# Optimization experiments

Hardware: AMD Instinct MI355X
Metric: run time of the kernel (lower is better)

Reference implementation:

```python
import jax, jax.numpy as jnp
import numpy as np

TOP_K = 6
N_GROUP = 4
TOPK_GROUP = 2
ROUTED_SCALING = 2.5

T, H, E, I = 1024, 2048, 16, 704  # tokens, hidden, experts, expert ffn width
IS = 2 * I  # shared expert intermediate (n_shared_experts * moe_intermediate_size)


def setup_inputs() -> dict:
    key = jax.random.key(0)
    ks = jax.random.split(key, 6)
    s = 0.02
    return {
        "hidden_states": jax.random.normal(ks[0], (T, H), jnp.float32),
        "w_gate": jax.random.normal(ks[1], (H, E), jnp.float32) * s,
        "w_gate_up": jax.random.normal(ks[2], (E, H, 2 * I), jnp.float32) * s,
        "w_down": jax.random.normal(ks[3], (E, I, H), jnp.float32) * s,
        "w_shared_gate_up": jax.random.normal(ks[4], (H, 2 * IS), jnp.float32) * s,
        "w_shared_down": jax.random.normal(ks[5], (IS, H), jnp.float32) * s,
    }


def grouped_topk(scores, k, n_group, topk_group):
    # DeepSeek grouped top-k routing: pick topk_group expert groups by max
    # group score, mask out other groups, then top-k over remaining experts.
    t, e = scores.shape
    group_scores = scores.reshape(t, n_group, e // n_group).max(axis=-1)  # [T, G]
    _, gidx = jax.lax.top_k(group_scores, topk_group)                     # [T, kg]
    gmask = jax.nn.one_hot(gidx, n_group, dtype=scores.dtype).sum(axis=1)  # [T, G]
    smask = jnp.repeat(gmask, e // n_group, axis=1)                        # [T, E]
    masked = jnp.where(smask > 0, scores, 0.0)
    topk_w, topk_idx = jax.lax.top_k(masked, k)                            # [T, k]
    topk_w = topk_w / jnp.sum(topk_w, axis=-1, keepdims=True)              # renormalize
    return topk_w, topk_idx


def reference(hidden_states, w_gate, w_gate_up, w_down, w_shared_gate_up, w_shared_down):
    x = hidden_states                         # [T, H]
    t, e = x.shape[0], w_gate.shape[1]
    # router
    router_logits = x @ w_gate                # [T, E]
    scores = jax.nn.softmax(router_logits, axis=-1)
    topk_w, topk_idx = grouped_topk(scores, TOP_K, N_GROUP, TOPK_GROUP)
    combine = jnp.zeros((t, e), x.dtype).at[jnp.arange(t)[:, None], topk_idx].add(topk_w)
    # routed experts (dense-all-experts form, mathematically identical to dispatch)
    gu = jnp.einsum('th,ehi->tei', x, w_gate_up)        # [T, E, 2I]
    g, u = jnp.split(gu, 2, axis=-1)
    act = jax.nn.silu(g) * u                            # [T, E, I]
    act = act * combine[:, :, None]                     # apply routing weights
    routed = jnp.einsum('tei,eih->th', act, w_down) * ROUTED_SCALING
    # shared experts (SiLU gated MLP)
    sgu = x @ w_shared_gate_up
    sg, su = jnp.split(sgu, 2, axis=-1)
    shared = (jax.nn.silu(sg) * su) @ w_shared_down
    return routed + shared
```

## Files before the change

kernel.cpp:

```cpp
#include <hip/hip_runtime.h>

typedef unsigned short u16;
typedef u16 u16x8 __attribute__((ext_vector_type(8)));
typedef __bf16 bf16x8 __attribute__((ext_vector_type(8)));
typedef float f32x4 __attribute__((ext_vector_type(4)));

#define T_TOK 1024
#define H_DIM 2048
#define E_NUM 16
#define I_DIM 704
#define IS_DIM 1408

#define MFMA(a, b, c) __builtin_amdgcn_mfma_f32_16x16x32_bf16(a, b, c, 0, 0, 0)

__device__ __forceinline__ u16 f2bf(float f) {
  union { float f; unsigned u; } v; v.f = f;
  unsigned r = v.u + 0x7fffu + ((v.u >> 16) & 1u);
  return (u16)(r >> 16);
}

__device__ __forceinline__ void gload16(const void* g, void* l) {
  __builtin_amdgcn_global_load_lds(
      (const __attribute__((address_space(1))) unsigned int*)g,
      (__attribute__((address_space(3))) unsigned int*)l, 16, 0, 0);
}

__device__ __forceinline__ const char* lds_sw(const u16* base, int row, int kByte) {
  return (const char*)base + row * 128 + (kByte ^ ((row & 7) << 4));
}

__device__ __forceinline__ void transp64_body(const float* __restrict__ in,
                                              u16* __restrict__ outp, int R, int C,
                                              int cx, int ry, int z, char* SM) {
  float (*tile)[65] = (float(*)[65])SM;
  const size_t base = (size_t)z * (size_t)R * C;
  const int c0 = cx * 64, r0 = ry * 64;
  const int tid = threadIdx.x;
  const int c4 = (tid & 15) * 4, rb = tid >> 4;
#pragma unroll
  for (int i = 0; i < 4; ++i) {
    const int row = i * 16 + rb;
    const f32x4 v = *(const f32x4*)(in + base + (size_t)(r0 + row) * C + c0 + c4);
    tile[row][c4 + 0] = v[0];
    tile[row][c4 + 1] = v[1];
    tile[row][c4 + 2] = v[2];
    tile[row][c4 + 3] = v[3];
  }
  __syncthreads();
#pragma unroll
  for (int i = 0; i < 8; ++i) {
    const int idx = i * 256 + tid;
    const int oc = idx >> 5, pr = idx & 31;
    const unsigned lo = f2bf(tile[2 * pr][oc]);
    const unsigned hi = f2bf(tile[2 * pr + 1][oc]);
    *(unsigned*)&outp[base + (size_t)(c0 + oc) * R + r0 + 2 * pr] = lo | (hi << 16);
  }
}

__global__ __launch_bounds__(256) void router_k(const float* __restrict__ x,
                                                const float* __restrict__ wg,
                                                float* __restrict__ comb,
                                                u16* __restrict__ XB) {
  const int t = blockIdx.x;
  const int tid = threadIdx.x;
  const float* xr = x + (size_t)t * H_DIM;
  const int h0 = tid * 8;
  f32x4 a = *(const f32x4*)(xr + h0);
  f32x4 b = *(const f32x4*)(xr + h0 + 4);
  u16x8 o;
  o[0] = f2bf(a[0]); o[1] = f2bf(a[1]); o[2] = f2bf(a[2]); o[3] = f2bf(a[3]);
  o[4] = f2bf(b[0]); o[5] = f2bf(b[1]); o[6] = f2bf(b[2]); o[7] = f2bf(b[3]);
  *(u16x8*)(XB + (size_t)t * H_DIM + h0) = o;

  float acc[E_NUM];
#pragma unroll
  for (int e = 0; e < E_NUM; ++e) acc[e] = 0.f;
#pragma unroll
  for (int j = 0; j < 8; ++j) {
    const float xv = j < 4 ? a[j] : b[j - 4];
    const f32x4* wr = (const f32x4*)(wg + (size_t)(h0 + j) * E_NUM);
#pragma unroll
    for (int q = 0; q < 4; ++q) {
      f32x4 w4 = wr[q];
      acc[q * 4 + 0] += xv * w4[0];
      acc[q * 4 + 1] += xv * w4[1];
      acc[q * 4 + 2] += xv * w4[2];
      acc[q * 4 + 3] += xv * w4[3];
    }
  }
#pragma unroll
  for (int e = 0; e < E_NUM; ++e)
    for (int off = 32; off > 0; off >>= 1) acc[e] += __shfl_down(acc[e], off);
  __shared__ float part[4][E_NUM];
  if ((tid & 63) == 0) {
#pragma unroll
    for (int e = 0; e < E_NUM; ++e) part[tid >> 6][e] = acc[e];
  }
  __syncthreads();
  if (tid == 0) {
    float p[E_NUM];
    float mx = -1e30f;
    for (int e = 0; e < E_NUM; ++e) {
      p[e] = part[0][e] + part[1][e] + part[2][e] + part[3][e];
      mx = fmaxf(mx, p[e]);
    }
    float s = 0.f;
    for (int e = 0; e < E_NUM; ++e) { p[e] = __expf(p[e] - mx); s += p[e]; }
    const float invs = 1.f / s;
    for (int e = 0; e < E_NUM; ++e) p[e] *= invs;
    float gs[4];
    for (int g = 0; g < 4; ++g)
      gs[g] = fmaxf(fmaxf(p[4 * g], p[4 * g + 1]), fmaxf(p[4 * g + 2], p[4 * g + 3]));
    int g1 = 0;
    for (int g = 1; g < 4; ++g) if (gs[g] > gs[g1]) g1 = g;
    int g2 = -1;
    for (int g = 0; g < 4; ++g) {
      if (g == g1) continue;
      if (g2 < 0 || gs[g] > gs[g2]) g2 = g;
    }
    float m2[E_NUM], cw[E_NUM];
    for (int e = 0; e < E_NUM; ++e) {
      int g = e >> 2;
      m2[e] = (g == g1 || g == g2) ? p[e] : 0.f;
      cw[e] = 0.f;
    }
    float sum6 = 0.f;
    for (int k = 0; k < 6; ++k) {
      int bi = 0; float bv = -1.f;
      for (int e = 0; e < E_NUM; ++e)
        if (m2[e] > bv) { bv = m2[e]; bi = e; }
      cw[bi] = bv; sum6 += bv; m2[bi] = -2.f;
    }
    const float scale = 2.5f / sum6;
    for (int e = 0; e < E_NUM; ++e) comb[t * E_NUM + e] = cw[e] * scale;
  }
}

__global__ __launch_bounds__(256) void dispatch_k(const float* __restrict__ comb,
                                                  int* __restrict__ cnt,
                                                  int* __restrict__ tok) {
  const int e = blockIdx.x;
  const int tid = threadIdx.x;
  const int lane = tid & 63, wid = tid >> 6;
  __shared__ int wtot[4];
  int running = 0;
  for (int chunk = 0; chunk < T_TOK / 256; ++chunk) {
    const int t = chunk * 256 + tid;
    const bool sel = comb[t * E_NUM + e] > 0.f;
    unsigned long long mask = __ballot(sel);
    const int pre = __popcll(mask & ((1ull << lane) - 1ull));
    if (lane == 0) wtot[wid] = __popcll(mask);
    __syncthreads();
    int wbase = running;
    for (int w = 0; w < wid; ++w) wbase += wtot[w];
    if (sel) tok[e * T_TOK + wbase + pre] = t;
    running += wtot[0] + wtot[1] + wtot[2] + wtot[3];
    __syncthreads();
  }
  if (tid == 0) cnt[e] = running;
}

#define TGU_WGU_BLKS (22 * 32 * 16)
__global__ __launch_bounds__(256) void transp_gu_k(const float* __restrict__ wgu,
                                                   const float* __restrict__ wsgu,
                                                   u16* __restrict__ WGUT,
                                                   u16* __restrict__ WSGUT) {
  __shared__ __align__(16) char SM[16640];
  const int bid = blockIdx.x;
  if (bid < TGU_WGU_BLKS) {
    transp64_body(wgu, WGUT, H_DIM, 2 * I_DIM, bid % 22, (bid / 22) % 32, bid / 704, SM);
  } else {
    const int id = bid - TGU_WGU_BLKS;
    transp64_body(wsgu, WSGUT, H_DIM, 2 * IS_DIM, id % 44, id / 44, 0, SM);
  }
}

__device__ __forceinline__ void gu_body(
    const u16* __restrict__ A, const u16* __restrict__ Bt,
    const float* __restrict__ comb, const int* __restrict__ cnt,
    const int* __restrict__ tok, u16* __restrict__ outp,
    int gu_off, long long bt_e_stride, long long out_e_stride, int out_stride,
    int bx, int by, int e, char* SM) {
  const int M = cnt ? cnt[e] : T_TOK;
  const int m0 = by * 128;
  if (m0 >= M) return;
  u16* S = (u16*)SM;
  int* tokS = (int*)(SM + 32768);

  const int n0 = bx * 64;
  const u16* Bte = Bt + (size_t)e * bt_e_stride;
  const u16* Bgp = Bte + (size_t)n0 * H_DIM;
  const u16* Bup = Bte + (size_t)(gu_off + n0) * H_DIM;
  const int tid = threadIdx.x;
  const int w = tid >> 6, l = tid & 63;
  const int r8 = l >> 3;
  const int sk = ((l & 7) ^ r8) * 8;

  if (tid < 128) {
    const int m = m0 + tid;
    const int mc = m < M ? m : M - 1;
    tokS[tid] = tok ? tok[e * T_TOK + mc] : mc;
  }
  size_t arow[4];
#pragma unroll
  for (int j = 0; j < 4; ++j) {
    const int m = m0 + w * 32 + j * 8 + r8;
    const int mc = m < M ? m : M - 1;
    const int t = tok ? tok[e * T_TOK + mc] : mc;
    arow[j] = (size_t)t * H_DIM + sk;
  }

  const int wr = tid >> 7;
  const int wc = (tid >> 6) & 1;
  const int fr = l & 15;
  const int fg = l >> 4;

  const f32x4 zero = {0.f, 0.f, 0.f, 0.f};
  f32x4 accg[4][2], accu[4][2];
#pragma unroll
  for (int i = 0; i < 4; ++i)
#pragma unroll
    for (int j = 0; j < 2; ++j) { accg[i][j] = zero; accu[i][j] = zero; }

  for (int kt = 0; kt < H_DIM / 64; ++kt) {
    const int k0 = kt * 64;
#pragma unroll
    for (int j = 0; j < 4; ++j)
      gload16(A + arow[j] + k0, S + (w * 4 + j) * 512);
#pragma unroll
    for (int j = 0; j < 2; ++j) {
      const size_t br = (size_t)(w * 16 + j * 8 + r8) * H_DIM + sk + k0;
      gload16(Bgp + br, S + 8192 + (w * 2 + j) * 512);
      gload16(Bup + br, S + 12288 + (w * 2 + j) * 512);
    }
    __syncthreads();
    const u16* AsC = S;
    const u16* BgC = S + 8192;
    const u16* BuC = S + 12288;
#pragma unroll
    for (int kk = 0; kk < 2; ++kk) {
      const int kb = kk * 64 + fg * 16;
      bf16x8 af[4], bg[2], bu[2];
#pragma unroll
      for (int mi = 0; mi < 4; ++mi)
        af[mi] = *(const bf16x8*)lds_sw(AsC, wr * 64 + mi * 16 + fr, kb);
#pragma unroll
      for (int ni = 0; ni < 2; ++ni) {
        bg[ni] = *(const bf16x8*)lds_sw(BgC, wc * 32 + ni * 16 + fr, kb);
        bu[ni] = *(const bf16x8*)lds_sw(BuC, wc * 32 + ni * 16 + fr, kb);
      }
#pragma unroll
      for (int mi = 0; mi < 4; ++mi)
#pragma unroll
        for (int ni = 0; ni < 2; ++ni) {
          accg[mi][ni] = MFMA(af[mi], bg[ni], accg[mi][ni]);
          accu[mi][ni] = MFMA(af[mi], bu[ni], accu[mi][ni]);
        }
    }
    __syncthreads();
  }

  const int colb = n0 + wc * 32;
#pragma unroll
  for (int mi = 0; mi < 4; ++mi) {
#pragma unroll
    for (int r = 0; r < 4; ++r) {
      const int ml = wr * 64 + mi * 16 + fg * 4 + r;
      if (m0 + ml >= M) continue;
      const float wgt = comb ? comb[tokS[ml] * E_NUM + e] : 1.0f;
      const size_t rowoff = (size_t)e * out_e_stride + (size_t)(m0 + ml) * out_stride;
#pragma unroll
      for (int ni = 0; ni < 2; ++ni) {
        float g = accg[mi][ni][r];
        float u = accu[mi][ni][r];
        float sg = g / (1.f + __expf(-g));
        outp[rowoff + colb + ni * 16 + fr] = f2bf(sg * u * wgt);
      }
    }
  }
}

#define MG_GUR_BLKS (11 * 8 * 16)
#define MG_GUS_BLKS (22 * 8)
#define MG_TWD_BLKS (32 * 11 * 16)
#define MG_TWSD_BLKS (32 * 22)
__global__ __launch_bounds__(256, 4) void mega_k(
    const u16* __restrict__ XB, const u16* __restrict__ WGUT,
    const u16* __restrict__ WSGUT, const float* __restrict__ comb,
    const int* __restrict__ cnt, const int* __restrict__ tok,
    u16* __restrict__ ACTC, u16* __restrict__ ACTS,
    const float* __restrict__ wd, const float* __restrict__ wsd,
    u16* __restrict__ WDT, u16* __restrict__ WSDT) {
  __shared__ __align__(16) char SM[33280];
  const int bid = blockIdx.x;
  if (bid < MG_GUR_BLKS) {
    gu_body(XB, WGUT, comb, cnt, tok, ACTC, I_DIM, (long long)(2 * I_DIM) * H_DIM,
            (long long)T_TOK * I_DIM, I_DIM, bid % 11, (bid / 11) % 8, bid / 88, SM);
  } else if (bid < MG_GUR_BLKS + MG_GUS_BLKS) {
    const int id = bid - MG_GUR_BLKS;
    gu_body(XB, WSGUT, nullptr, nullptr, nullptr, ACTS, IS_DIM, 0, 0, IS_DIM,
            id % 22, id / 22, 0, SM);
  } else if (bid < MG_GUR_BLKS + MG_GUS_BLKS + MG_TWD_BLKS) {
    const int id = bid - MG_GUR_BLKS - MG_GUS_BLKS;
    transp64_body(wd, WDT, I_DIM, H_DIM, id % 32, (id / 32) % 11, id / 352, SM);
  } else {
    const int id = bid - MG_GUR_BLKS - MG_GUS_BLKS - MG_TWD_BLKS;
    transp64_body(wsd, WSDT, IS_DIM, H_DIM, id % 32, id / 32, 0, SM);
  }
}

template <bool ATOMIC>
__device__ __forceinline__ void down_core(
    const u16* __restrict__ Ap, int astride,
    const u16* __restrict__ Bp, int bstride,
    int NT, int M, int m0, int n0, const int* tokS, float* __restrict__ outp) {
  __shared__ __align__(16) u16 S[12288];
  const int tid = threadIdx.x;
  const int w = tid >> 6, l = tid & 63;
  const int r8 = l >> 3;
  const int sk = ((l & 7) ^ r8) * 8;

  size_t arow[2];
#pragma unroll
  for (int j = 0; j < 2; ++j) {
    const int m = w * 16 + j * 8 + r8;
    arow[j] = (size_t)(m0 + m < M ? m : (M - 1 - m0 > 0 ? M - 1 - m0 : 0)) * astride + sk;
  }
  size_t brow[4];
#pragma unroll
  for (int j = 0; j < 4; ++j)
    brow[j] = (size_t)(w * 32 + j * 8 + r8) * bstride + sk;

  auto STAGE = [&](int kt) {
    const int k0 = kt * 64;
#pragma unroll
    for (int j = 0; j < 2; ++j)
      gload16(Ap + arow[j] + k0, S + (w * 2 + j) * 512);
#pragma unroll
    for (int j = 0; j < 4; ++j)
      gload16(Bp + brow[j] + k0, S + 4096 + (w * 4 + j) * 512);
  };

  const int fr = l & 15, fg = l >> 4;
  const f32x4 zero = {0.f, 0.f, 0.f, 0.f};
  f32x4 acc[4][2];
#pragma unroll
  for (int i = 0; i < 4; ++i)
#pragma unroll
    for (int j = 0; j < 2; ++j) acc[i][j] = zero;

  for (int kt = 0; kt < NT; ++kt) {
    STAGE(kt);
    __syncthreads();
    const u16* AsC = S;
    const u16* BsC = S + 4096;
#pragma unroll
    for (int kk = 0; kk < 2; ++kk) {
      const int kb = kk * 64 + fg * 16;
      bf16x8 af[4], bfr[2];
#pragma unroll
      for (int mi = 0; mi < 4; ++mi)
        af[mi] = *(const bf16x8*)lds_sw(AsC, mi * 16 + fr, kb);
#pragma unroll
      for (int ni = 0; ni < 2; ++ni)
        bfr[ni] = *(const bf16x8*)lds_sw(BsC, w * 32 + ni * 16 + fr, kb);
#pragma unroll
      for (int mi = 0; mi < 4; ++mi)
#pragma unroll
        for (int ni = 0; ni < 2; ++ni) acc[mi][ni] = MFMA(af[mi], bfr[ni], acc[mi][ni]);
    }
    __syncthreads();
  }

#pragma unroll
  for (int mi = 0; mi < 4; ++mi) {
#pragma unroll
    for (int r = 0; r < 4; ++r) {
      const int ml = mi * 16 + fg * 4 + r;
      if (m0 + ml >= M) continue;
      const int trow = ATOMIC ? tokS[ml] : (m0 + ml);
      float* op = outp + (size_t)trow * H_DIM + n0 + w * 32;
#pragma unroll
      for (int ni = 0; ni < 2; ++ni) {
        if (ATOMIC)
          atomicAdd(op + ni * 16 + fr, acc[mi][ni][r]);
        else
          op[ni * 16 + fr] = acc[mi][ni][r];
      }
    }
  }
}

__global__ __launch_bounds__(256, 4) void down_shared_k(
    const u16* __restrict__ A1, const u16* __restrict__ B1t, float* __restrict__ outp) {
  const int n0 = blockIdx.x * 128, m0 = blockIdx.y * 64;
  down_core<false>(A1 + (size_t)m0 * IS_DIM, IS_DIM, B1t + (size_t)n0 * IS_DIM, IS_DIM,
                   IS_DIM / 64, T_TOK, m0, n0, nullptr, outp);
}

__global__ __launch_bounds__(256, 4) void down_routed_k(
    const u16* __restrict__ ACTC, const u16* __restrict__ WDT,
    const int* __restrict__ cnt, const int* __restrict__ tok, float* __restrict__ outp) {
  const int e = blockIdx.z;
  const int M = cnt[e];
  const int m0 = blockIdx.y * 64;
  if (m0 >= M) return;
  const int n0 = blockIdx.x * 128;
  __shared__ int tokS[64];
  const int tid = threadIdx.x;
  if (tid < 64) tokS[tid] = tok[e * T_TOK + (m0 + tid < M ? m0 + tid : M - 1)];
  __syncthreads();
  down_core<true>(ACTC + ((size_t)e * T_TOK + m0) * I_DIM, I_DIM,
                  WDT + ((size_t)e * H_DIM + n0) * I_DIM, I_DIM,
                  I_DIM / 64, M, m0, n0, tokS, outp);
}

extern "C" void kernel_launch(void* const* d_in, const int* in_sizes, int n_in,
                              void* d_out, int out_size, void* d_ws, size_t ws_size,
                              hipStream_t stream) {
  const float* x    = (const float*)d_in[0];
  const float* wg   = (const float*)d_in[1];
  const float* wgu  = (const float*)d_in[2];
  const float* wd   = (const float*)d_in[3];
  const float* wsgu = (const float*)d_in[4];
  const float* wsd  = (const float*)d_in[5];
  float* out = (float*)d_out;

  char* ws = (char*)d_ws;
  size_t off = 0;
  auto alloc = [&](size_t b) { size_t r = off; off += (b + 255) & ~(size_t)255; return r; };
  u16*   XB    = (u16*)  (ws + alloc((size_t)T_TOK * H_DIM * 2));
  float* COMB  = (float*)(ws + alloc((size_t)T_TOK * E_NUM * 4));
  int*   CNT   = (int*)  (ws + alloc((size_t)E_NUM * 4));
  int*   TOK   = (int*)  (ws + alloc((size_t)E_NUM * T_TOK * 4));
  u16*   WGUT  = (u16*)  (ws + alloc((size_t)E_NUM * 2 * I_DIM * H_DIM * 2));
  u16*   WDT   = (u16*)  (ws + alloc((size_t)E_NUM * H_DIM * I_DIM * 2));
  u16*   WSGUT = (u16*)  (ws + alloc((size_t)2 * IS_DIM * H_DIM * 2));
  u16*   WSDT  = (u16*)  (ws + alloc((size_t)H_DIM * IS_DIM * 2));
  u16*   ACTC  = (u16*)  (ws + alloc((size_t)E_NUM * T_TOK * I_DIM * 2));
  u16*   ACTS  = (u16*)  (ws + alloc((size_t)T_TOK * IS_DIM * 2));
  if (ws_size < off) return;

  router_k<<<T_TOK, 256, 0, stream>>>(x, wg, COMB, XB);
  dispatch_k<<<E_NUM, 256, 0, stream>>>(COMB, CNT, TOK);
  transp_gu_k<<<TGU_WGU_BLKS + 32 * 44, 256, 0, stream>>>(wgu, wsgu, WGUT, WSGUT);
  mega_k<<<MG_GUR_BLKS + MG_GUS_BLKS + MG_TWD_BLKS + MG_TWSD_BLKS, 256, 0, stream>>>(
      XB, WGUT, WSGUT, COMB, CNT, TOK, ACTC, ACTS, wd, wsd, WDT, WSDT);
  down_shared_k<<<dim3(H_DIM / 128, T_TOK / 64), 256, 0, stream>>>(ACTS, WSDT, out);
  down_routed_k<<<dim3(H_DIM / 128, T_TOK / 64, E_NUM), 256, 0, stream>>>(
      ACTC, WDT, CNT, TOK, out);
}
```

Before: 258.3 us.

## Interleave GEMM and transpose blocks in mega kernel and raise occupancy bounds

The fused mega kernel now interleaves its blocks: one gate/up GEMM block is followed by four weight-transpose blocks. Before, all GEMM blocks ran first and then all transpose blocks, so the intent is to overlap compute-bound and memory-bound work on each CU. The shared token-index LDS buffer is removed, with routing weights looked up straight from global memory, so LDS drops to 32 KB. Launch bounds go up to 5 blocks per SM for the mega kernel and 6 for the down kernels. The higher bounds may force register spills, and the extra global index loads add latency in the epilogue.

```diff
diff --git a/kernel.cpp b/kernel.cpp
--- a/kernel.cpp
+++ b/kernel.cpp
@@ -185,7 +185,6 @@
   const int m0 = by * 128;
   if (m0 >= M) return;
   u16* S = (u16*)SM;
-  int* tokS = (int*)(SM + 32768);
 
   const int n0 = bx * 64;
   const u16* Bte = Bt + (size_t)e * bt_e_stride;
@@ -196,11 +195,6 @@
   const int r8 = l >> 3;
   const int sk = ((l & 7) ^ r8) * 8;
 
-  if (tid < 128) {
-    const int m = m0 + tid;
-    const int mc = m < M ? m : M - 1;
-    tokS[tid] = tok ? tok[e * T_TOK + mc] : mc;
-  }
   size_t arow[4];
 #pragma unroll
   for (int j = 0; j < 4; ++j) {
@@ -267,7 +261,8 @@
     for (int r = 0; r < 4; ++r) {
       const int ml = wr * 64 + mi * 16 + fg * 4 + r;
       if (m0 + ml >= M) continue;
-      const float wgt = comb ? comb[tokS[ml] * E_NUM + e] : 1.0f;
+      const int trow = tok ? tok[e * T_TOK + m0 + ml] : (m0 + ml);
+      const float wgt = comb ? comb[trow * E_NUM + e] : 1.0f;
       const size_t rowoff = (size_t)e * out_e_stride + (size_t)(m0 + ml) * out_stride;
 #pragma unroll
       for (int ni = 0; ni < 2; ++ni) {
@@ -284,28 +279,33 @@
 #define MG_GUS_BLKS (22 * 8)
 #define MG_TWD_BLKS (32 * 11 * 16)
 #define MG_TWSD_BLKS (32 * 22)
-__global__ __launch_bounds__(256, 4) void mega_k(
+__global__ __launch_bounds__(256, 5) void mega_k(
     const u16* __restrict__ XB, const u16* __restrict__ WGUT,
     const u16* __restrict__ WSGUT, const float* __restrict__ comb,
     const int* __restrict__ cnt, const int* __restrict__ tok,
     u16* __restrict__ ACTC, u16* __restrict__ ACTS,
     const float* __restrict__ wd, const float* __restrict__ wsd,
     u16* __restrict__ WDT, u16* __restrict__ WSDT) {
-  __shared__ __align__(16) char SM[33280];
+  __shared__ __align__(16) char SM[32768];
   const int bid = blockIdx.x;
-  if (bid < MG_GUR_BLKS) {
-    gu_body(XB, WGUT, comb, cnt, tok, ACTC, I_DIM, (long long)(2 * I_DIM) * H_DIM,
-            (long long)T_TOK * I_DIM, I_DIM, bid % 11, (bid / 11) % 8, bid / 88, SM);
-  } else if (bid < MG_GUR_BLKS + MG_GUS_BLKS) {
-    const int id = bid - MG_GUR_BLKS;
-    gu_body(XB, WSGUT, nullptr, nullptr, nullptr, ACTS, IS_DIM, 0, 0, IS_DIM,
-            id % 22, id / 22, 0, SM);
-  } else if (bid < MG_GUR_BLKS + MG_GUS_BLKS + MG_TWD_BLKS) {
-    const int id = bid - MG_GUR_BLKS - MG_GUS_BLKS;
-    transp64_body(wd, WDT, I_DIM, H_DIM, id % 32, (id / 32) % 11, id / 352, SM);
+  const int g = bid / 5, r = bid % 5;
+  if (r == 0) {
+    if (g < MG_GUR_BLKS) {
+      gu_body(XB, WGUT, comb, cnt, tok, ACTC, I_DIM, (long long)(2 * I_DIM) * H_DIM,
+              (long long)T_TOK * I_DIM, I_DIM, g % 11, (g / 11) % 8, g / 88, SM);
+    } else {
+      const int id = g - MG_GUR_BLKS;
+      gu_body(XB, WSGUT, nullptr, nullptr, nullptr, ACTS, IS_DIM, 0, 0, IS_DIM,
+              id % 22, id / 22, 0, SM);
+    }
   } else {
-    const int id = bid - MG_GUR_BLKS - MG_GUS_BLKS - MG_TWD_BLKS;
-    transp64_body(wsd, WSDT, IS_DIM, H_DIM, id % 32, id / 32, 0, SM);
+    const int t = g * 4 + (r - 1);
+    if (t < MG_TWD_BLKS) {
+      transp64_body(wd, WDT, I_DIM, H_DIM, t % 32, (t / 32) % 11, t / 352, SM);
+    } else {
+      const int id = t - MG_TWD_BLKS;
+      transp64_body(wsd, WSDT, IS_DIM, H_DIM, id % 32, id / 32, 0, SM);
+    }
   }
 }
 
@@ -391,14 +391,14 @@
   }
 }
 
-__global__ __launch_bounds__(256, 4) void down_shared_k(
+__global__ __launch_bounds__(256, 6) void down_shared_k(
     const u16* __restrict__ A1, const u16* __restrict__ B1t, float* __restrict__ outp) {
   const int n0 = blockIdx.x * 128, m0 = blockIdx.y * 64;
   down_core<false>(A1 + (size_t)m0 * IS_DIM, IS_DIM, B1t + (size_t)n0 * IS_DIM, IS_DIM,
                    IS_DIM / 64, T_TOK, m0, n0, nullptr, outp);
 }
 
-__global__ __launch_bounds__(256, 4) void down_routed_k(
+__global__ __launch_bounds__(256, 6) void down_routed_k(
     const u16* __restrict__ ACTC, const u16* __restrict__ WDT,
     const int* __restrict__ cnt, const int* __restrict__ tok, float* __restrict__ outp) {
   const int e = blockIdx.z;
@@ -444,7 +444,7 @@
   router_k<<<T_TOK, 256, 0, stream>>>(x, wg, COMB, XB);
   dispatch_k<<<E_NUM, 256, 0, stream>>>(COMB, CNT, TOK);
   transp_gu_k<<<TGU_WGU_BLKS + 32 * 44, 256, 0, stream>>>(wgu, wsgu, WGUT, WSGUT);
-  mega_k<<<MG_GUR_BLKS + MG_GUS_BLKS + MG_TWD_BLKS + MG_TWSD_BLKS, 256, 0, stream>>>(
+  mega_k<<<(MG_GUR_BLKS + MG_GUS_BLKS + MG_TWD_BLKS + MG_TWSD_BLKS), 256, 0, stream>>>(
       XB, WGUT, WSGUT, COMB, CNT, TOK, ACTC, ACTS, wd, wsd, WDT, WSDT);
   down_shared_k<<<dim3(H_DIM / 128, T_TOK / 64), 256, 0, stream>>>(ACTS, WSDT, out);
   down_routed_k<<<dim3(H_DIM / 128, T_TOK / 64, E_NUM), 256, 0, stream>>>(
```

Result: slower. 329.2 us (+27.5%).
